# Performance work log

Measured on AMD Instinct MI355X. Metric: run time of the kernel, lower is better.

Reference implementation:

```python
import jax, jax.numpy as jnp
import numpy as np

D_MODEL = 1024
N_HEADS = 16
HEAD_DIM = D_MODEL // N_HEADS


def setup_inputs() -> dict:
    key = jax.random.key(0)
    k_x, k_qkv, k_out = jax.random.split(key, 3)
    B, T = 4, 2048
    x = jax.random.normal(k_x, (B, T, D_MODEL), dtype=jnp.float32)
    # Linear(bias=False): y = x @ W, with W stored as [in, out]
    W_qkv = jax.random.normal(k_qkv, (D_MODEL, 3 * D_MODEL), dtype=jnp.float32) * (D_MODEL ** -0.5)
    W_out = jax.random.normal(k_out, (D_MODEL, D_MODEL), dtype=jnp.float32) * (D_MODEL ** -0.5)
    return {"x": x, "W_qkv": W_qkv, "W_out": W_out}


def reference(x, W_qkv, W_out):
    B, T, C = x.shape
    H, Dh = N_HEADS, HEAD_DIM
    scale = 1.0 / jnp.sqrt(jnp.asarray(Dh, dtype=x.dtype))

    qkv = x @ W_qkv  # [B,T,3C]
    q, k, v = jnp.split(qkv, 3, axis=-1)

    def split_heads(t):
        return t.reshape(B, T, H, Dh).transpose(0, 2, 1, 3)  # [B,H,T,Dh]

    q, k, v = split_heads(q), split_heads(k), split_heads(v)

    scores = jnp.einsum('bhqd,bhkd->bhqk', q, k) * scale  # [B,H,T,T]
    causal = jnp.tril(jnp.ones((T, T), dtype=bool))
    scores = jnp.where(causal, scores, jnp.asarray(-jnp.inf, dtype=scores.dtype))
    attn = jax.nn.softmax(scores, axis=-1)
    # dropout p=0.0 -> identity
    out = jnp.einsum('bhqk,bhkd->bhqd', attn, v)  # [B,H,T,Dh]
    out = out.transpose(0, 2, 1, 3).reshape(B, T, C)
    return out @ W_out
```

## Files before the change

### kernel.cpp

```cpp
#include <hip/hip_runtime.h>
#include <stdint.h>

typedef unsigned short u16;
typedef float f32x4 __attribute__((ext_vector_type(4)));
typedef short s16x8 __attribute__((ext_vector_type(8)));

#define SEQ 2048
#define DM 1024
#define NH 16
#define HD 64
#define BATCH 4
#define ROWS (BATCH*SEQ)
#define QTILES (SEQ/64)

__device__ __forceinline__ u16 f32_bf16(float f) {
  union { float f; uint32_t u; } c; c.f = f;
  uint32_t u = c.u;
  return (u16)((u + 0x7fffu + ((u >> 16) & 1u)) >> 16);
}
__device__ __forceinline__ u16 f32_bf16_trunc(float f) {
  union { float f; uint32_t u; } c; c.f = f;
  return (u16)(c.u >> 16);
}

#define GLOAD_LDS16(g, l) __builtin_amdgcn_global_load_lds( \
    (__attribute__((address_space(1))) void*)(g),           \
    (__attribute__((address_space(3))) void*)(l), 16, 0, 0)

__global__ __launch_bounds__(256) void cast_bf16_k(const float* __restrict__ in,
                                                   u16* __restrict__ out, int n4) {
  int i = blockIdx.x * 256 + threadIdx.x;
  if (i >= n4) return;
  float4 v = ((const float4*)in)[i];
  ushort4 o;
  o.x = f32_bf16(v.x); o.y = f32_bf16(v.y); o.z = f32_bf16(v.z); o.w = f32_bf16(v.w);
  ((ushort4*)out)[i] = o;
}

__global__ __launch_bounds__(256) void cast_transpose_k(const float* __restrict__ in,
                                                        u16* __restrict__ out, int R, int C) {
  __shared__ float tile[32][33];
  int c0 = blockIdx.x * 32, r0 = blockIdx.y * 32;
  int t = threadIdx.x;
  int lr = t >> 3, lc = (t & 7) * 4;
  float4 v = *(const float4*)(in + (size_t)(r0 + lr) * C + c0 + lc);
  tile[lr][lc] = v.x; tile[lr][lc + 1] = v.y; tile[lr][lc + 2] = v.z; tile[lr][lc + 3] = v.w;
  __syncthreads();
  ushort4 o;
  o.x = f32_bf16(tile[lc + 0][lr]);
  o.y = f32_bf16(tile[lc + 1][lr]);
  o.z = f32_bf16(tile[lc + 2][lr]);
  o.w = f32_bf16(tile[lc + 3][lr]);
  *(ushort4*)(out + (size_t)(c0 + lr) * R + r0 + lc) = o;
}

#define QSCALE 0.18033688011112042f

template<int EPI, int TM>
__global__ __launch_bounds__(256) void gemm_bt(
    const u16* __restrict__ A, const u16* __restrict__ Bt,
    float* __restrict__ Cf, u16* __restrict__ Qo, u16* __restrict__ Ko, u16* __restrict__ Vo,
    int M, int N, int K)
{
  constexpr int NI = (TM == 128) ? 4 : 2;
  __shared__ u16 As[TM * 32];
  __shared__ u16 Bs[128 * 32];
  int t = threadIdx.x;
  int m0 = blockIdx.y * TM, n0 = blockIdx.x * 128;

  int srow = t >> 2, scol8 = (t & 3) * 8;
  const u16* Ag0 = A  + (size_t)(m0 + srow) * K + scol8;
  const u16* Ag1 = A  + (size_t)(m0 + 64 + srow) * K + scol8;
  const u16* Bg0 = Bt + (size_t)(n0 + srow) * K + scol8;
  const u16* Bg1 = Bt + (size_t)(n0 + 64 + srow) * K + scol8;
  u16* Al0 = As + t * 8;  u16* Al1 = As + 2048 + t * 8;
  u16* Bl0 = Bs + t * 8;  u16* Bl1 = Bs + 2048 + t * 8;

  int lane = t & 63, w = t >> 6;
  int m16 = lane & 15, quad = lane >> 4;
  int wr = (TM == 128) ? (w >> 1) * 64 : 0;
  int wc = (TM == 128) ? (w & 1) * 64 : w * 32;

  f32x4 acc[4][NI];
#pragma unroll
  for (int mi = 0; mi < 4; ++mi)
#pragma unroll
    for (int ni = 0; ni < NI; ++ni)
#pragma unroll
      for (int r = 0; r < 4; ++r) acc[mi][ni][r] = 0.f;

  for (int k0 = 0; k0 < K; k0 += 32) {
    __syncthreads();
    GLOAD_LDS16(Ag0 + k0, Al0);
    if (TM == 128) GLOAD_LDS16(Ag1 + k0, Al1);
    GLOAD_LDS16(Bg0 + k0, Bl0);
    GLOAD_LDS16(Bg1 + k0, Bl1);
    __syncthreads();
    s16x8 af[4], bf[NI];
#pragma unroll
    for (int mi = 0; mi < 4; ++mi)
      af[mi] = *(const s16x8*)(As + (wr + mi * 16 + m16) * 32 + quad * 8);
#pragma unroll
    for (int ni = 0; ni < NI; ++ni)
      bf[ni] = *(const s16x8*)(Bs + (wc + ni * 16 + m16) * 32 + quad * 8);
#pragma unroll
    for (int mi = 0; mi < 4; ++mi)
#pragma unroll
      for (int ni = 0; ni < NI; ++ni)
        acc[mi][ni] = __builtin_amdgcn_mfma_f32_16x16x32_bf16(af[mi], bf[ni], acc[mi][ni], 0, 0, 0);
  }

  if (EPI == 0) {
#pragma unroll
    for (int mi = 0; mi < 4; ++mi) {
      int gr = m0 + wr + mi * 16 + quad * 4;
#pragma unroll
      for (int ni = 0; ni < NI; ++ni) {
        int gc = n0 + wc + ni * 16 + m16;
#pragma unroll
        for (int r = 0; r < 4; ++r)
          Cf[(size_t)(gr + r) * N + gc] = acc[mi][ni][r];
      }
    }
  } else {
#pragma unroll
    for (int mi = 0; mi < 4; ++mi) {
      int gr = m0 + wr + mi * 16 + quad * 4;
      int b = gr >> 11, tt = gr & 2047;
#pragma unroll
      for (int ni = 0; ni < NI; ++ni) {
        int gc = n0 + wc + ni * 16 + m16;
        int sec = gc >> 10, rem = gc & 1023, h = rem >> 6, d = rem & 63;
        if (sec == 0) {
#pragma unroll
          for (int r = 0; r < 4; ++r)
            Qo[(((size_t)b * NH + h) * SEQ + tt + r) * HD + d] = f32_bf16(acc[mi][ni][r] * QSCALE);
        } else if (sec == 1) {
#pragma unroll
          for (int r = 0; r < 4; ++r)
            Ko[(((size_t)b * NH + h) * SEQ + tt + r) * HD + d] = f32_bf16(acc[mi][ni][r]);
        } else {
          ushort4 o;
          o.x = f32_bf16(acc[mi][ni][0]); o.y = f32_bf16(acc[mi][ni][1]);
          o.z = f32_bf16(acc[mi][ni][2]); o.w = f32_bf16(acc[mi][ni][3]);
          *(ushort4*)&Vo[(((size_t)b * NH + h) * HD + d) * SEQ + tt] = o;
        }
      }
    }
  }
}

__global__ __launch_bounds__(256) void attn_k(
    const u16* __restrict__ Q, const u16* __restrict__ K,
    const u16* __restrict__ Vt_g,
    u16* __restrict__ O)
{
  __shared__ u16 Ks[64][72];
  __shared__ u16 Vt[64][72];
  __shared__ u16 Ps[4][16][72];
  int bh = blockIdx.y;
  int t = threadIdx.x, w = t >> 6, lane = t & 63;
  int m16 = lane & 15, quad = lane >> 4;
  int b = bh >> 4, h = bh & 15;

  int srow = t >> 2, sc = (t & 3) * 16;
  const u16* Kg0 = K    + ((size_t)bh * SEQ + srow) * HD  + sc;
  const u16* Vg0 = Vt_g + ((size_t)bh * HD  + srow) * SEQ + sc;

  for (int half = 0; half < 2; ++half) {
    int qt = half ? (QTILES - 1 - (int)blockIdx.x) : (int)blockIdx.x;
    int q0 = qt * 64;

    const u16* Qb = Q + ((size_t)bh * SEQ + q0 + w * 16 + m16) * HD + quad * 8;
    s16x8 qf0 = *(const s16x8*)Qb;
    s16x8 qf1 = *(const s16x8*)(Qb + 32);

    f32x4 acco[4];
    float l_part[4];
#pragma unroll
    for (int r = 0; r < 4; ++r) l_part[r] = 0.f;
#pragma unroll
    for (int ni = 0; ni < 4; ++ni)
#pragma unroll
      for (int r = 0; r < 4; ++r) acco[ni][r] = 0.f;

    for (int kt = 0; kt <= qt; ++kt) {
      uint4 kv0 = *(const uint4*)(Kg0 + (size_t)kt * 64 * HD);
      uint4 kv1 = *(const uint4*)(Kg0 + (size_t)kt * 64 * HD + 8);
      uint4 vv0 = *(const uint4*)(Vg0 + kt * 64);
      uint4 vv1 = *(const uint4*)(Vg0 + kt * 64 + 8);
      __syncthreads();
      *(uint4*)&Ks[srow][sc]     = kv0;
      *(uint4*)&Ks[srow][sc + 8] = kv1;
      *(uint4*)&Vt[srow][sc]     = vv0;
      *(uint4*)&Vt[srow][sc + 8] = vv1;
      __syncthreads();

      f32x4 sacc[4];
#pragma unroll
      for (int ni = 0; ni < 4; ++ni)
#pragma unroll
        for (int r = 0; r < 4; ++r) sacc[ni][r] = 0.f;
#pragma unroll
      for (int ni = 0; ni < 4; ++ni) {
        s16x8 kf0 = *(const s16x8*)&Ks[ni * 16 + m16][quad * 8];
        s16x8 kf1 = *(const s16x8*)&Ks[ni * 16 + m16][32 + quad * 8];
        sacc[ni] = __builtin_amdgcn_mfma_f32_16x16x32_bf16(qf0, kf0, sacc[ni], 0, 0, 0);
        sacc[ni] = __builtin_amdgcn_mfma_f32_16x16x32_bf16(qf1, kf1, sacc[ni], 0, 0, 0);
      }
      if (kt == qt) {
#pragma unroll
        for (int ni = 0; ni < 4; ++ni)
#pragma unroll
          for (int r = 0; r < 4; ++r)
            if (ni * 16 + m16 > w * 16 + quad * 4 + r) sacc[ni][r] = -1e30f;
      }

#pragma unroll
      for (int ni = 0; ni < 4; ++ni)
#pragma unroll
        for (int r = 0; r < 4; ++r) {
          float p = __builtin_amdgcn_exp2f(sacc[ni][r]);
          l_part[r] += p;
          Ps[w][quad * 4 + r][ni * 16 + m16] = f32_bf16_trunc(p);
        }

#pragma unroll
      for (int ks = 0; ks < 2; ++ks) {
        s16x8 pf = *(const s16x8*)&Ps[w][m16][ks * 32 + quad * 8];
#pragma unroll
        for (int ni = 0; ni < 4; ++ni) {
          s16x8 vf = *(const s16x8*)&Vt[ni * 16 + m16][ks * 32 + quad * 8];
          acco[ni] = __builtin_amdgcn_mfma_f32_16x16x32_bf16(pf, vf, acco[ni], 0, 0, 0);
        }
      }
    }

    float l[4];
#pragma unroll
    for (int r = 0; r < 4; ++r) l[r] = l_part[r];
#pragma unroll
    for (int off = 1; off < 16; off <<= 1)
#pragma unroll
      for (int r = 0; r < 4; ++r) l[r] += __shfl_xor(l[r], off, 64);

#pragma unroll
    for (int r = 0; r < 4; ++r) {
      float inv = 1.f / l[r];
      int trow = q0 + w * 16 + quad * 4 + r;
      size_t base = ((size_t)(b * SEQ + trow)) * DM + h * HD;
#pragma unroll
      for (int ni = 0; ni < 4; ++ni)
        O[base + ni * 16 + m16] = f32_bf16(acco[ni][r] * inv);
    }
  }
}

extern "C" void kernel_launch(void* const* d_in, const int* in_sizes, int n_in,
                              void* d_out, int out_size, void* d_ws, size_t ws_size,
                              hipStream_t stream) {
  const float* x    = (const float*)d_in[0];
  const float* Wqkv = (const float*)d_in[1];
  const float* Wout = (const float*)d_in[2];
  float* out = (float*)d_out;

  u16* ws = (u16*)d_ws;
  size_t off = 0;
  u16* x_bf   = ws + off; off += (size_t)ROWS * DM;
  u16* wqkv_t = ws + off; off += (size_t)(3 * DM) * DM;
  u16* wout_t = ws + off; off += (size_t)DM * DM;
  u16* Qb     = ws + off; off += (size_t)BATCH * NH * SEQ * HD;
  u16* Kb     = ws + off; off += (size_t)BATCH * NH * SEQ * HD;
  u16* Vb     = ws + off; off += (size_t)BATCH * NH * SEQ * HD;
  u16* AO     = ws + off; off += (size_t)ROWS * DM;

  cast_bf16_k<<<(ROWS * DM / 4 + 255) / 256, 256, 0, stream>>>(x, x_bf, ROWS * DM / 4);
  cast_transpose_k<<<dim3(3 * DM / 32, DM / 32), 256, 0, stream>>>(Wqkv, wqkv_t, DM, 3 * DM);
  cast_transpose_k<<<dim3(DM / 32, DM / 32), 256, 0, stream>>>(Wout, wout_t, DM, DM);
  gemm_bt<1, 128><<<dim3(3 * DM / 128, ROWS / 128), 256, 0, stream>>>(
      x_bf, wqkv_t, nullptr, Qb, Kb, Vb, ROWS, 3 * DM, DM);
  attn_k<<<dim3(QTILES / 2, BATCH * NH), 256, 0, stream>>>(Qb, Kb, Vb, AO);
  gemm_bt<0, 64><<<dim3(DM / 128, ROWS / 64), 256, 0, stream>>>(
      AO, wout_t, out, nullptr, nullptr, nullptr, ROWS, DM, DM);
}
```

Measured before the change: 288.1 us.

## Compute transposed S=K·Qᵀ so P stays in registers, dropping LDS round-trip

The attention kernel swaps the MFMA operand order so the score tile is produced transposed (keys along rows, queries along lanes). Each lane's exp'd probabilities can then be packed directly into the B operand of the PV MFMA, which removes the per-warp Ps shared-memory buffer, its stores and reloads. The row-sum reduction shrinks to two shuffles and the output becomes vectorized ushort4 stores. In exchange, V fragments are now read as two 4-element LDS loads instead of one 8-element load, and the register packing adds some permute instructions.

```diff
diff --git a/kernel.cpp b/kernel.cpp
--- a/kernel.cpp
+++ b/kernel.cpp
@@ -157,7 +157,6 @@
 {
   __shared__ u16 Ks[64][72];
   __shared__ u16 Vt[64][72];
-  __shared__ u16 Ps[4][16][72];
   int bh = blockIdx.y;
   int t = threadIdx.x, w = t >> 6, lane = t & 63;
   int m16 = lane & 15, quad = lane >> 4;
@@ -176,13 +175,11 @@
     s16x8 qf1 = *(const s16x8*)(Qb + 32);
 
     f32x4 acco[4];
-    float l_part[4];
-#pragma unroll
-    for (int r = 0; r < 4; ++r) l_part[r] = 0.f;
-#pragma unroll
-    for (int ni = 0; ni < 4; ++ni)
-#pragma unroll
-      for (int r = 0; r < 4; ++r) acco[ni][r] = 0.f;
+    float l_part = 0.f;
+#pragma unroll
+    for (int mi = 0; mi < 4; ++mi)
+#pragma unroll
+      for (int r = 0; r < 4; ++r) acco[mi][r] = 0.f;
 
     for (int kt = 0; kt <= qt; ++kt) {
       uint4 kv0 = *(const uint4*)(Kg0 + (size_t)kt * 64 * HD);
@@ -198,60 +195,65 @@
 
       f32x4 sacc[4];
 #pragma unroll
-      for (int ni = 0; ni < 4; ++ni)
+      for (int ni = 0; ni < 4; ++ni) {
 #pragma unroll
         for (int r = 0; r < 4; ++r) sacc[ni][r] = 0.f;
-#pragma unroll
-      for (int ni = 0; ni < 4; ++ni) {
         s16x8 kf0 = *(const s16x8*)&Ks[ni * 16 + m16][quad * 8];
         s16x8 kf1 = *(const s16x8*)&Ks[ni * 16 + m16][32 + quad * 8];
-        sacc[ni] = __builtin_amdgcn_mfma_f32_16x16x32_bf16(qf0, kf0, sacc[ni], 0, 0, 0);
-        sacc[ni] = __builtin_amdgcn_mfma_f32_16x16x32_bf16(qf1, kf1, sacc[ni], 0, 0, 0);
+        sacc[ni] = __builtin_amdgcn_mfma_f32_16x16x32_bf16(kf0, qf0, sacc[ni], 0, 0, 0);
+        sacc[ni] = __builtin_amdgcn_mfma_f32_16x16x32_bf16(kf1, qf1, sacc[ni], 0, 0, 0);
       }
       if (kt == qt) {
 #pragma unroll
         for (int ni = 0; ni < 4; ++ni)
 #pragma unroll
           for (int r = 0; r < 4; ++r)
-            if (ni * 16 + m16 > w * 16 + quad * 4 + r) sacc[ni][r] = -1e30f;
-      }
-
+            if (ni * 16 + quad * 4 + r > w * 16 + m16) sacc[ni][r] = -1e30f;
+      }
+
+      u16 pe[16];
 #pragma unroll
       for (int ni = 0; ni < 4; ++ni)
 #pragma unroll
         for (int r = 0; r < 4; ++r) {
           float p = __builtin_amdgcn_exp2f(sacc[ni][r]);
-          l_part[r] += p;
-          Ps[w][quad * 4 + r][ni * 16 + m16] = f32_bf16_trunc(p);
-        }
-
-#pragma unroll
-      for (int ks = 0; ks < 2; ++ks) {
-        s16x8 pf = *(const s16x8*)&Ps[w][m16][ks * 32 + quad * 8];
-#pragma unroll
-        for (int ni = 0; ni < 4; ++ni) {
-          s16x8 vf = *(const s16x8*)&Vt[ni * 16 + m16][ks * 32 + quad * 8];
-          acco[ni] = __builtin_amdgcn_mfma_f32_16x16x32_bf16(pf, vf, acco[ni], 0, 0, 0);
-        }
-      }
-    }
-
-    float l[4];
-#pragma unroll
-    for (int r = 0; r < 4; ++r) l[r] = l_part[r];
-#pragma unroll
-    for (int off = 1; off < 16; off <<= 1)
-#pragma unroll
-      for (int r = 0; r < 4; ++r) l[r] += __shfl_xor(l[r], off, 64);
-
-#pragma unroll
-    for (int r = 0; r < 4; ++r) {
-      float inv = 1.f / l[r];
-      int trow = q0 + w * 16 + quad * 4 + r;
-      size_t base = ((size_t)(b * SEQ + trow)) * DM + h * HD;
-#pragma unroll
-      for (int ni = 0; ni < 4; ++ni)
-        O[base + ni * 16 + m16] = f32_bf16(acco[ni][r] * inv);
+          l_part += p;
+          pe[ni * 4 + r] = f32_bf16_trunc(p);
+        }
+
+#pragma unroll
+      for (int g = 0; g < 2; ++g) {
+        union { s16x8 v; u16 e[8]; } pf;
+#pragma unroll
+        for (int r = 0; r < 4; ++r) {
+          pf.e[r]     = pe[(2 * g) * 4 + r];
+          pf.e[4 + r] = pe[(2 * g + 1) * 4 + r];
+        }
+#pragma unroll
+        for (int mi = 0; mi < 4; ++mi) {
+          union { s16x8 v; ushort4 h[2]; } vf;
+          vf.h[0] = *(const ushort4*)&Vt[mi * 16 + m16][g * 32 + quad * 4];
+          vf.h[1] = *(const ushort4*)&Vt[mi * 16 + m16][g * 32 + 16 + quad * 4];
+          acco[mi] = __builtin_amdgcn_mfma_f32_16x16x32_bf16(vf.v, pf.v, acco[mi], 0, 0, 0);
+        }
+      }
+    }
+
+    float l = l_part;
+    l += __shfl_xor(l, 16, 64);
+    l += __shfl_xor(l, 32, 64);
+    float inv = 1.f / l;
+
+    int trow = q0 + w * 16 + m16;
+    size_t base = ((size_t)(b * SEQ + trow)) * DM + h * HD;
+#pragma unroll
+    for (int mi = 0; mi < 4; ++mi) {
+      ushort4 o;
+      o.x = f32_bf16(acco[mi][0] * inv);
+      o.y = f32_bf16(acco[mi][1] * inv);
+      o.z = f32_bf16(acco[mi][2] * inv);
+      o.w = f32_bf16(acco[mi][3] * inv);
+      *(ushort4*)&O[base + mi * 16 + quad * 4] = o;
     }
   }
 }
```

After: 295.6 us. +2.6%, slower.
